# Kernel optimization log

Measured on AMD Instinct MI355X. Metric: run time of the kernel, lower is better.

## Reference

```python
import jax, jax.numpy as jnp
import numpy as np

D_MODEL, N_HEADS = 512, 8
HEAD_DIM = D_MODEL // N_HEADS
LN_EPS = 1e-5


def setup_inputs() -> dict:
    key = jax.random.key(0)
    ks = jax.random.split(key, 6)
    b, n = 8, 1024
    x = jax.random.normal(ks[0], (b, n, D_MODEL), dtype=jnp.float32)
    W_qkv = jax.random.normal(ks[1], (D_MODEL, 3 * D_MODEL), dtype=jnp.float32) * (1.0 / np.sqrt(D_MODEL))
    b_qkv = jnp.zeros((3 * D_MODEL,), dtype=jnp.float32)
    reattn_w = jax.random.normal(ks[2], (N_HEADS, N_HEADS), dtype=jnp.float32)
    ln_g = jnp.ones((N_HEADS,), dtype=jnp.float32)
    ln_b = jnp.zeros((N_HEADS,), dtype=jnp.float32)
    W_out = jax.random.normal(ks[3], (D_MODEL, D_MODEL), dtype=jnp.float32) * (1.0 / np.sqrt(D_MODEL))
    b_out = jnp.zeros((D_MODEL,), dtype=jnp.float32)
    return {"x": x, "W_qkv": W_qkv, "b_qkv": b_qkv, "reattn_w": reattn_w,
            "ln_g": ln_g, "ln_b": ln_b, "W_out": W_out, "b_out": b_out}


def reference(x, W_qkv, b_qkv, reattn_w, ln_g, ln_b, W_out, b_out):
    b, n, _ = x.shape
    scale = jnp.float32(HEAD_DIM ** -0.5)  # lsa=False -> non-trainable constant
    qkv = x @ W_qkv + b_qkv                                  # (b, n, 3*d_model)
    q, k, v = jnp.split(qkv, 3, axis=-1)
    def to_heads(t):  # b n (h d) -> b h n d
        return t.reshape(b, n, N_HEADS, HEAD_DIM).transpose(0, 2, 1, 3)
    q, k, v = to_heads(q), to_heads(k), to_heads(v)
    scores = jnp.einsum('bhid,bhjd->bhij', q, k) * scale      # (b, h, n, n)
    attn = jax.nn.softmax(scores, axis=-1)
    # cross-head re-attention mix
    attn = jnp.einsum('bhij,hk->bkij', attn, reattn_w)
    # LayerNorm over the head axis (axis=1)
    mu = jnp.mean(attn, axis=1, keepdims=True)
    var = jnp.var(attn, axis=1, keepdims=True)
    attn = (attn - mu) * jax.lax.rsqrt(var + LN_EPS)
    attn = attn * ln_g[None, :, None, None] + ln_b[None, :, None, None]
    out = jnp.einsum('bhij,bhjd->bhid', attn, v)              # (b, h, n, d)
    out = out.transpose(0, 2, 1, 3).reshape(b, n, D_MODEL)    # b n (h d)
    out = out @ W_out + b_out
    return (out, attn)
```

## Files before the change

### kernel.cpp

```cpp
#include <hip/hip_runtime.h>

#define SCALE_ 0.125f
#define LN_EPS_ 1e-5f

typedef __attribute__((ext_vector_type(8))) short bf16x8;
typedef __attribute__((ext_vector_type(4))) float f32x4;

__device__ __forceinline__ ushort f2b(float f) {
  union { float f; unsigned u; } x; x.f = f;
  unsigned r = x.u + 0x7FFFu + ((x.u >> 16) & 1u);
  return (ushort)(r >> 16);
}

__device__ __forceinline__ f32x4 mfma16(bf16x8 a, bf16x8 b, f32x4 c) {
  return __builtin_amdgcn_mfma_f32_16x16x32_bf16(a, b, c, 0, 0, 0);
}

__device__ __forceinline__ void bar_lds() {
  asm volatile("s_waitcnt lgkmcnt(0)\n\ts_barrier" ::: "memory");
  __builtin_amdgcn_sched_barrier(0);
}

__global__ __launch_bounds__(256) void cast_transpose(const float* __restrict__ src,
                                                      ushort* __restrict__ dst,
                                                      int R, int C) {
  __shared__ ushort t[64][65];
  const int tid = threadIdx.x;
  const int c0 = blockIdx.x * 64, r0 = blockIdx.y * 64;
  const int lr = tid >> 2, lc = (tid & 3) * 16;
#pragma unroll
  for (int u = 0; u < 4; ++u) {
    float4 v = *(const float4*)&src[(size_t)(r0 + lr) * C + c0 + lc + u * 4];
    t[lc + u * 4 + 0][lr] = f2b(v.x);
    t[lc + u * 4 + 1][lr] = f2b(v.y);
    t[lc + u * 4 + 2][lr] = f2b(v.z);
    t[lc + u * 4 + 3][lr] = f2b(v.w);
  }
  __syncthreads();
#pragma unroll
  for (int u = 0; u < 2; ++u) {
    bf16x8 o;
#pragma unroll
    for (int e = 0; e < 8; ++e) o[e] = (short)t[lr][lc + u * 8 + e];
    *(bf16x8*)&dst[(size_t)(c0 + lr) * R + r0 + lc + u * 8] = o;
  }
}

__global__ __launch_bounds__(256) void qkv_mfma(const float* __restrict__ x,
                                                const ushort* __restrict__ Wt,
                                                const float* __restrict__ bias,
                                                ushort* __restrict__ q,
                                                ushort* __restrict__ k,
                                                ushort* __restrict__ vt) {
  __shared__ ushort A[128][40];
  __shared__ ushort Bs[128][40];
  const int tid = threadIdx.x;
  const int n0 = blockIdx.x * 128;
  const int m0 = blockIdx.y * 128;
  const int lane = tid & 63, wid = tid >> 6;
  const int wr = wid >> 1, wc = wid & 1;
  const int lr = lane & 15, g4 = lane >> 4;
  const int sr = tid >> 1, sco = (tid & 1) * 16;
  f32x4 acc[4][4] = {};
  for (int k0 = 0; k0 < 512; k0 += 32) {
    {
      const float4* xs = (const float4*)&x[(size_t)(m0 + sr) * 512 + k0 + sco];
      float4 v0 = xs[0], v1 = xs[1], v2 = xs[2], v3 = xs[3];
      bf16x8 p0, p1;
      p0[0] = (short)f2b(v0.x); p0[1] = (short)f2b(v0.y);
      p0[2] = (short)f2b(v0.z); p0[3] = (short)f2b(v0.w);
      p0[4] = (short)f2b(v1.x); p0[5] = (short)f2b(v1.y);
      p0[6] = (short)f2b(v1.z); p0[7] = (short)f2b(v1.w);
      p1[0] = (short)f2b(v2.x); p1[1] = (short)f2b(v2.y);
      p1[2] = (short)f2b(v2.z); p1[3] = (short)f2b(v2.w);
      p1[4] = (short)f2b(v3.x); p1[5] = (short)f2b(v3.y);
      p1[6] = (short)f2b(v3.z); p1[7] = (short)f2b(v3.w);
      *(bf16x8*)&A[sr][sco] = p0;
      *(bf16x8*)&A[sr][sco + 8] = p1;
    }
    {
      const bf16x8* wp = (const bf16x8*)&Wt[(size_t)(n0 + sr) * 512 + k0 + sco];
      *(bf16x8*)&Bs[sr][sco] = wp[0];
      *(bf16x8*)&Bs[sr][sco + 8] = wp[1];
    }
    __syncthreads();
    bf16x8 af[4], bf[4];
#pragma unroll
    for (int mr = 0; mr < 4; ++mr) af[mr] = *(bf16x8*)&A[wr * 64 + mr * 16 + lr][g4 * 8];
#pragma unroll
    for (int nr = 0; nr < 4; ++nr) bf[nr] = *(bf16x8*)&Bs[wc * 64 + nr * 16 + lr][g4 * 8];
#pragma unroll
    for (int mr = 0; mr < 4; ++mr)
#pragma unroll
      for (int nr = 0; nr < 4; ++nr) acc[mr][nr] = mfma16(af[mr], bf[nr], acc[mr][nr]);
    __syncthreads();
  }
  const int part = n0 >> 9;
#pragma unroll
  for (int mr = 0; mr < 4; ++mr)
#pragma unroll
    for (int nr = 0; nr < 4; ++nr) {
      const int n = n0 + wc * 64 + nr * 16 + lr;
      const int h = (n & 511) >> 6, d = n & 63;
      const float bb = bias[n];
#pragma unroll
      for (int r = 0; r < 4; ++r) {
        int token = m0 + wr * 64 + mr * 16 + g4 * 4 + r;
        int bi = token >> 10, ii = token & 1023;
        ushort valb = f2b(acc[mr][nr][r] + bb);
        if (part == 0)
          q[(((size_t)(bi * 8 + h) * 1024 + ii) * 64) + d] = valb;
        else if (part == 1)
          k[(((size_t)(bi * 8 + h) * 1024 + ii) * 64) + d] = valb;
        else
          vt[((size_t)(bi * 8 + h) * 64 + d) * 1024 + ii] = valb;
      }
    }
}

__global__ __launch_bounds__(512, 2) void attn_fused(const ushort* __restrict__ q,
                                                     const ushort* __restrict__ k,
                                                     const ushort* __restrict__ vt,
                                                     const float* __restrict__ rw,
                                                     const float* __restrict__ ln_g,
                                                     const float* __restrict__ ln_b,
                                                     float* __restrict__ attn,
                                                     ushort* __restrict__ pv) {
  __shared__ float PM[8][32][36];
  __shared__ float wsh[64];
  __shared__ float gsh[8], bsh[8];

  const int tid = threadIdx.x;
  const int lane = tid & 63;
  const int h = tid >> 6;
  const int obid = ((blockIdx.x & 7) << 5) + (blockIdx.x >> 3);
  const int i0 = (obid & 31) * 32;
  const int b = obid >> 5;
  const int lr = lane & 15, g4 = lane >> 4;

  const ushort* qh = q + ((size_t)(b * 8 + h) * 1024 + i0) * 64;
  const ushort* kh = k + (size_t)(b * 8 + h) * 65536;
  const ushort* vth = vt + (size_t)(b * 8 + h) * 65536;

  if (tid < 64) wsh[tid] = rw[tid];
  if (tid < 8) { gsh[tid] = ln_g[tid]; bsh[tid] = ln_b[tid]; }

  bf16x8 qf[2][2];
#pragma unroll
  for (int mr = 0; mr < 2; ++mr)
#pragma unroll
    for (int ks = 0; ks < 2; ++ks)
      qf[mr][ks] = *(const bf16x8*)&qh[(size_t)(mr * 16 + lr) * 64 + ks * 32 + g4 * 8];

  float psum[2][4] = {};
  {
    bf16x8 kc[4], kn[4];
#pragma unroll
    for (int nr = 0; nr < 2; ++nr)
#pragma unroll
      for (int ks = 0; ks < 2; ++ks)
        kc[nr * 2 + ks] = *(const bf16x8*)&kh[(size_t)(nr * 16 + lr) * 64 + ks * 32 + g4 * 8];
    for (int jt = 0; jt < 32; ++jt) {
      const int j0n = ((jt + 1) & 31) * 32;
#pragma unroll
      for (int nr = 0; nr < 2; ++nr)
#pragma unroll
        for (int ks = 0; ks < 2; ++ks)
          kn[nr * 2 + ks] =
              *(const bf16x8*)&kh[(size_t)(j0n + nr * 16 + lr) * 64 + ks * 32 + g4 * 8];
      f32x4 sa[2][2] = {};
#pragma unroll
      for (int mr = 0; mr < 2; ++mr)
#pragma unroll
        for (int nr = 0; nr < 2; ++nr) {
          sa[mr][nr] = mfma16(qf[mr][0], kc[nr * 2 + 0], sa[mr][nr]);
          sa[mr][nr] = mfma16(qf[mr][1], kc[nr * 2 + 1], sa[mr][nr]);
        }
#pragma unroll
      for (int mr = 0; mr < 2; ++mr)
#pragma unroll
        for (int nr = 0; nr < 2; ++nr)
#pragma unroll
          for (int r = 0; r < 4; ++r) psum[mr][r] += __expf(sa[mr][nr][r] * SCALE_);
#pragma unroll
      for (int i = 0; i < 4; ++i) kc[i] = kn[i];
    }
  }
  float inv_[2][4];
#pragma unroll
  for (int mr = 0; mr < 2; ++mr)
#pragma unroll
    for (int r = 0; r < 4; ++r) {
      float s = psum[mr][r];
#pragma unroll
      for (int off = 1; off <= 8; off <<= 1) s += __shfl_xor(s, off);
      inv_[mr][r] = 1.0f / s;
    }

  f32x4 oacc[2][4] = {};
  const int pair = tid & 1, chunk = tid >> 1;
  const int m_ii = chunk >> 3, m_jj = (chunk & 7) * 4;
  const int k2base = pair * 4;

  bf16x8 kc[4], kn[4];
#pragma unroll
  for (int nr = 0; nr < 2; ++nr)
#pragma unroll
    for (int ks = 0; ks < 2; ++ks)
      kc[nr * 2 + ks] = *(const bf16x8*)&kh[(size_t)(nr * 16 + lr) * 64 + ks * 32 + g4 * 8];

  for (int jt = 0; jt < 32; ++jt) {
    const int j0 = jt * 32;
    const int j0n = ((jt + 1) & 31) * 32;
#pragma unroll
    for (int nr = 0; nr < 2; ++nr)
#pragma unroll
      for (int ks = 0; ks < 2; ++ks)
        kn[nr * 2 + ks] =
            *(const bf16x8*)&kh[(size_t)(j0n + nr * 16 + lr) * 64 + ks * 32 + g4 * 8];

    f32x4 sa[2][2] = {};
#pragma unroll
    for (int mr = 0; mr < 2; ++mr)
#pragma unroll
      for (int nr = 0; nr < 2; ++nr) {
        sa[mr][nr] = mfma16(qf[mr][0], kc[nr * 2 + 0], sa[mr][nr]);
        sa[mr][nr] = mfma16(qf[mr][1], kc[nr * 2 + 1], sa[mr][nr]);
      }
#pragma unroll
    for (int mr = 0; mr < 2; ++mr)
#pragma unroll
      for (int nr = 0; nr < 2; ++nr)
#pragma unroll
        for (int r = 0; r < 4; ++r)
          PM[h][mr * 16 + g4 * 4 + r][nr * 16 + lr] =
              __expf(sa[mr][nr][r] * SCALE_) * inv_[mr][r];

    bf16x8 vc[4];
#pragma unroll
    for (int nd = 0; nd < 4; ++nd)
      vc[nd] = *(const bf16x8*)&vth[(size_t)(nd * 16 + lr) * 1024 + j0 + g4 * 8];

    bar_lds();

    float4 ph[8];
#pragma unroll
    for (int h2 = 0; h2 < 8; ++h2) ph[h2] = *(const float4*)&PM[h2][m_ii][m_jj];
    float mixed[4][4];
#pragma unroll
    for (int k2l = 0; k2l < 4; ++k2l) {
      float a0 = 0.f, a1 = 0.f, a2 = 0.f, a3 = 0.f;
#pragma unroll
      for (int h2 = 0; h2 < 8; ++h2) {
        float w = wsh[h2 * 8 + k2base + k2l];
        a0 += ph[h2].x * w; a1 += ph[h2].y * w;
        a2 += ph[h2].z * w; a3 += ph[h2].w * w;
      }
      mixed[k2l][0] = a0; mixed[k2l][1] = a1; mixed[k2l][2] = a2; mixed[k2l][3] = a3;
    }
    float mu[4], rs_[4];
#pragma unroll
    for (int e = 0; e < 4; ++e) {
      float mp = mixed[0][e] + mixed[1][e] + mixed[2][e] + mixed[3][e];
      mu[e] = (mp + __shfl_xor(mp, 1)) * 0.125f;
    }
#pragma unroll
    for (int e = 0; e < 4; ++e) {
      float vp = 0.f;
#pragma unroll
      for (int k2l = 0; k2l < 4; ++k2l) {
        float d = mixed[k2l][e] - mu[e];
        vp += d * d;
      }
      float var = (vp + __shfl_xor(vp, 1)) * 0.125f;
      rs_[e] = rsqrtf(var + LN_EPS_);
    }
#pragma unroll
    for (int k2l = 0; k2l < 4; ++k2l) {
      int k2 = k2base + k2l;
      float g = gsh[k2], be = bsh[k2];
      f32x4 o;
      o[0] = (mixed[k2l][0] - mu[0]) * rs_[0] * g + be;
      o[1] = (mixed[k2l][1] - mu[1]) * rs_[1] * g + be;
      o[2] = (mixed[k2l][2] - mu[2]) * rs_[2] * g + be;
      o[3] = (mixed[k2l][3] - mu[3]) * rs_[3] * g + be;
      __builtin_nontemporal_store(
          o, (f32x4*)&attn[((size_t)(b * 8 + k2) << 20) + ((size_t)(i0 + m_ii) << 10) +
                           j0 + m_jj]);
      *(f32x4*)&PM[k2][m_ii][m_jj] = o;
    }

    bar_lds();

    bf16x8 pa[2];
#pragma unroll
    for (int mr = 0; mr < 2; ++mr) {
      const float* pr = &PM[h][mr * 16 + lr][g4 * 8];
      float4 p0 = *(const float4*)&pr[0];
      float4 p1 = *(const float4*)&pr[4];
      bf16x8 t;
      t[0] = (short)f2b(p0.x); t[1] = (short)f2b(p0.y);
      t[2] = (short)f2b(p0.z); t[3] = (short)f2b(p0.w);
      t[4] = (short)f2b(p1.x); t[5] = (short)f2b(p1.y);
      t[6] = (short)f2b(p1.z); t[7] = (short)f2b(p1.w);
      pa[mr] = t;
    }
#pragma unroll
    for (int nd = 0; nd < 4; ++nd) {
      oacc[0][nd] = mfma16(pa[0], vc[nd], oacc[0][nd]);
      oacc[1][nd] = mfma16(pa[1], vc[nd], oacc[1][nd]);
    }

#pragma unroll
    for (int i = 0; i < 4; ++i) kc[i] = kn[i];
  }

  ushort* po = pv + ((size_t)(b * 8 + h) * 1024 + i0) * 64;
#pragma unroll
  for (int mr = 0; mr < 2; ++mr)
#pragma unroll
    for (int nd = 0; nd < 4; ++nd)
#pragma unroll
      for (int r = 0; r < 4; ++r)
        po[(size_t)(mr * 16 + g4 * 4 + r) * 64 + nd * 16 + lr] = f2b(oacc[mr][nd][r]);
}

__global__ __launch_bounds__(256) void out_mfma(const ushort* __restrict__ pvb,
                                                const ushort* __restrict__ Wt,
                                                const float* __restrict__ bias,
                                                float* __restrict__ out) {
  __shared__ ushort A[128][40];
  __shared__ ushort Bs[128][40];
  const int tid = threadIdx.x;
  const int n0 = blockIdx.x * 128;
  const int m0 = blockIdx.y * 128;
  const int lane = tid & 63, wid = tid >> 6;
  const int wr = wid >> 1, wc = wid & 1;
  const int lr = lane & 15, g4 = lane >> 4;
  const int sr = tid >> 1, sco = (tid & 1) * 16;
  f32x4 acc[4][4] = {};
  for (int k0 = 0; k0 < 512; k0 += 32) {
    {
      int token = m0 + sr;
      int bi = token >> 10, ii = token & 1023;
      int f = k0 + sco;
      int hh = f >> 6, d = f & 63;
      const bf16x8* src =
          (const bf16x8*)&pvb[(((size_t)(bi * 8 + hh)) * 1024 + ii) * 64 + d];
      *(bf16x8*)&A[sr][sco] = src[0];
      *(bf16x8*)&A[sr][sco + 8] = src[1];
    }
    {
      const bf16x8* wp = (const bf16x8*)&Wt[(size_t)(n0 + sr) * 512 + k0 + sco];
      *(bf16x8*)&Bs[sr][sco] = wp[0];
      *(bf16x8*)&Bs[sr][sco + 8] = wp[1];
    }
    __syncthreads();
    bf16x8 af[4], bf[4];
#pragma unroll
    for (int mr = 0; mr < 4; ++mr) af[mr] = *(bf16x8*)&A[wr * 64 + mr * 16 + lr][g4 * 8];
#pragma unroll
    for (int nr = 0; nr < 4; ++nr) bf[nr] = *(bf16x8*)&Bs[wc * 64 + nr * 16 + lr][g4 * 8];
#pragma unroll
    for (int mr = 0; mr < 4; ++mr)
#pragma unroll
      for (int nr = 0; nr < 4; ++nr) acc[mr][nr] = mfma16(af[mr], bf[nr], acc[mr][nr]);
    __syncthreads();
  }
#pragma unroll
  for (int mr = 0; mr < 4; ++mr)
#pragma unroll
    for (int nr = 0; nr < 4; ++nr) {
      const int n = n0 + wc * 64 + nr * 16 + lr;
      const float bb = bias[n];
#pragma unroll
      for (int r = 0; r < 4; ++r) {
        int token = m0 + wr * 64 + mr * 16 + g4 * 4 + r;
        out[(size_t)token * 512 + n] = acc[mr][nr][r] + bb;
      }
    }
}

extern "C" void kernel_launch(void* const* d_in, const int* in_sizes, int n_in,
                              void* d_out, int out_size, void* d_ws, size_t ws_size,
                              hipStream_t stream) {
  const float* x    = (const float*)d_in[0];
  const float* Wqkv = (const float*)d_in[1];
  const float* bqkv = (const float*)d_in[2];
  const float* rw   = (const float*)d_in[3];
  const float* lng  = (const float*)d_in[4];
  const float* lnb  = (const float*)d_in[5];
  const float* Wout = (const float*)d_in[6];
  const float* bout = (const float*)d_in[7];

  float* out  = (float*)d_out;
  float* attn = (float*)d_out + 4194304;

  char* wsb = (char*)d_ws;
  ushort* q     = (ushort*)(wsb);
  ushort* k     = (ushort*)(wsb + (8u << 20));
  ushort* vt    = (ushort*)(wsb + (16u << 20));
  ushort* pvb   = (ushort*)(wsb + (24u << 20));
  ushort* Wqkvt = (ushort*)(wsb + (32u << 20));
  ushort* Woutt = (ushort*)(wsb + (33u << 20) + (1u << 19));

  cast_transpose<<<dim3(24, 8), 256, 0, stream>>>(Wqkv, Wqkvt, 512, 1536);
  cast_transpose<<<dim3(8, 8), 256, 0, stream>>>(Wout, Woutt, 512, 512);

  qkv_mfma<<<dim3(12, 64), 256, 0, stream>>>(x, Wqkvt, bqkv, q, k, vt);
  attn_fused<<<dim3(256), 512, 0, stream>>>(q, k, vt, rw, lng, lnb, attn, pvb);
  out_mfma<<<dim3(4, 64), 256, 0, stream>>>(pvb, Woutt, bout, out);
}
```

Before: 183.6 us.

## Split softmax denominators into separate kernel and halve attention key range per block

Moves the softmax row-sum pass out of the fused attention kernel into a new small kernel that writes per-row inverse denominators. The fused kernel then only does one pass over half the key range per block, doubling the grid to 512 blocks. The two partial P·V results go to separate bf16 buffers that out_mfma sums on load. It also transposes the MFMA operand order for vectorized LDS and global stores and uses a packed bf16 conversion. This targets the low block count of the old grid and the duplicated QK^T pass. The cost is an extra launch, extra workspace traffic, and an added bf16 rounding from summing two partial results.

```diff
diff --git a/kernel.cpp b/kernel.cpp
--- a/kernel.cpp
+++ b/kernel.cpp
@@ -1,4 +1,5 @@
 #include <hip/hip_runtime.h>
+#include <hip/hip_bf16.h>
 
 #define SCALE_ 0.125f
 #define LN_EPS_ 1e-5f
@@ -10,6 +11,14 @@
   union { float f; unsigned u; } x; x.f = f;
   unsigned r = x.u + 0x7FFFu + ((x.u >> 16) & 1u);
   return (ushort)(r >> 16);
+}
+__device__ __forceinline__ float b2f(short s) {
+  union { float f; unsigned u; } x; x.u = ((unsigned)(ushort)s) << 16; return x.f;
+}
+__device__ __forceinline__ unsigned cvtpk(float lo, float hi) {
+  union { __hip_bfloat162 h; unsigned u; } x;
+  x.h = __float22bfloat162_rn(make_float2(lo, hi));
+  return x.u;
 }
 
 __device__ __forceinline__ f32x4 mfma16(bf16x8 a, bf16x8 b, f32x4 c) {
@@ -118,14 +127,80 @@
     }
 }
 
-__global__ __launch_bounds__(512, 2) void attn_fused(const ushort* __restrict__ q,
+__global__ __launch_bounds__(64) void denoms(const ushort* __restrict__ q,
+                                             const ushort* __restrict__ k,
+                                             float* __restrict__ invg) {
+  const int bid = blockIdx.x;
+  const int obid = ((bid & 7) << 8) + (bid >> 3);
+  const int bh = obid >> 5;
+  const int it = obid & 31;
+  const int lane = threadIdx.x;
+  const int lr = lane & 15, g4 = lane >> 4;
+  const ushort* qh = q + ((size_t)bh * 1024 + it * 32) * 64;
+  const ushort* kh = k + (size_t)bh * 65536;
+
+  bf16x8 qf[2][2];
+#pragma unroll
+  for (int ir = 0; ir < 2; ++ir)
+#pragma unroll
+    for (int ks = 0; ks < 2; ++ks)
+      qf[ir][ks] = *(const bf16x8*)&qh[(size_t)(ir * 16 + lr) * 64 + ks * 32 + g4 * 8];
+
+  float psum[2] = {0.f, 0.f};
+  bf16x8 kc[4], kn[4];
+#pragma unroll
+  for (int jr = 0; jr < 2; ++jr)
+#pragma unroll
+    for (int ks = 0; ks < 2; ++ks)
+      kc[jr * 2 + ks] = *(const bf16x8*)&kh[(size_t)(jr * 16 + lr) * 64 + ks * 32 + g4 * 8];
+  for (int jt = 0; jt < 32; ++jt) {
+    const int j0n = ((jt + 1) & 31) * 32;
+#pragma unroll
+    for (int jr = 0; jr < 2; ++jr)
+#pragma unroll
+      for (int ks = 0; ks < 2; ++ks)
+        kn[jr * 2 + ks] =
+            *(const bf16x8*)&kh[(size_t)(j0n + jr * 16 + lr) * 64 + ks * 32 + g4 * 8];
+    f32x4 sa[2][2] = {};
+#pragma unroll
+    for (int jr = 0; jr < 2; ++jr)
+#pragma unroll
+      for (int ir = 0; ir < 2; ++ir) {
+        sa[jr][ir] = mfma16(kc[jr * 2 + 0], qf[ir][0], sa[jr][ir]);
+        sa[jr][ir] = mfma16(kc[jr * 2 + 1], qf[ir][1], sa[jr][ir]);
+      }
+#pragma unroll
+    for (int jr = 0; jr < 2; ++jr)
+#pragma unroll
+      for (int ir = 0; ir < 2; ++ir)
+#pragma unroll
+        for (int r = 0; r < 4; ++r) psum[ir] += __expf(sa[jr][ir][r] * SCALE_);
+#pragma unroll
+    for (int i = 0; i < 4; ++i) kc[i] = kn[i];
+  }
+#pragma unroll
+  for (int ir = 0; ir < 2; ++ir) {
+    float s = psum[ir];
+    s += __shfl_xor(s, 16);
+    s += __shfl_xor(s, 32);
+    psum[ir] = s;
+  }
+  if (lane < 16) {
+    invg[(size_t)bh * 1024 + it * 32 + lr] = 1.0f / psum[0];
+    invg[(size_t)bh * 1024 + it * 32 + 16 + lr] = 1.0f / psum[1];
+  }
+}
+
+__global__ __launch_bounds__(512, 4) void attn_fused(const ushort* __restrict__ q,
                                                      const ushort* __restrict__ k,
                                                      const ushort* __restrict__ vt,
                                                      const float* __restrict__ rw,
                                                      const float* __restrict__ ln_g,
                                                      const float* __restrict__ ln_b,
+                                                     const float* __restrict__ invg,
                                                      float* __restrict__ attn,
-                                                     ushort* __restrict__ pv) {
+                                                     ushort* __restrict__ pv0,
+                                                     ushort* __restrict__ pv1) {
   __shared__ float PM[8][32][36];
   __shared__ float wsh[64];
   __shared__ float gsh[8], bsh[8];
@@ -133,113 +208,71 @@
   const int tid = threadIdx.x;
   const int lane = tid & 63;
   const int h = tid >> 6;
-  const int obid = ((blockIdx.x & 7) << 5) + (blockIdx.x >> 3);
-  const int i0 = (obid & 31) * 32;
-  const int b = obid >> 5;
+  const int obid = ((blockIdx.x & 7) << 6) + (blockIdx.x >> 3);
+  const int b = obid >> 6;
+  const int rem = obid & 63;
+  const int i0 = (rem & 31) * 32;
+  const int jh = rem >> 5;
+  const int jbase = jh * 512;
   const int lr = lane & 15, g4 = lane >> 4;
 
-  const ushort* qh = q + ((size_t)(b * 8 + h) * 1024 + i0) * 64;
-  const ushort* kh = k + (size_t)(b * 8 + h) * 65536;
-  const ushort* vth = vt + (size_t)(b * 8 + h) * 65536;
+  const int bh = b * 8 + h;
+  const ushort* qh = q + ((size_t)bh * 1024 + i0) * 64;
+  const ushort* kh = k + (size_t)bh * 65536;
+  const ushort* vth = vt + (size_t)bh * 65536;
 
   if (tid < 64) wsh[tid] = rw[tid];
   if (tid < 8) { gsh[tid] = ln_g[tid]; bsh[tid] = ln_b[tid]; }
 
   bf16x8 qf[2][2];
 #pragma unroll
-  for (int mr = 0; mr < 2; ++mr)
+  for (int ir = 0; ir < 2; ++ir)
 #pragma unroll
     for (int ks = 0; ks < 2; ++ks)
-      qf[mr][ks] = *(const bf16x8*)&qh[(size_t)(mr * 16 + lr) * 64 + ks * 32 + g4 * 8];
-
-  float psum[2][4] = {};
-  {
-    bf16x8 kc[4], kn[4];
-#pragma unroll
-    for (int nr = 0; nr < 2; ++nr)
-#pragma unroll
-      for (int ks = 0; ks < 2; ++ks)
-        kc[nr * 2 + ks] = *(const bf16x8*)&kh[(size_t)(nr * 16 + lr) * 64 + ks * 32 + g4 * 8];
-    for (int jt = 0; jt < 32; ++jt) {
-      const int j0n = ((jt + 1) & 31) * 32;
-#pragma unroll
-      for (int nr = 0; nr < 2; ++nr)
-#pragma unroll
-        for (int ks = 0; ks < 2; ++ks)
-          kn[nr * 2 + ks] =
-              *(const bf16x8*)&kh[(size_t)(j0n + nr * 16 + lr) * 64 + ks * 32 + g4 * 8];
-      f32x4 sa[2][2] = {};
-#pragma unroll
-      for (int mr = 0; mr < 2; ++mr)
-#pragma unroll
-        for (int nr = 0; nr < 2; ++nr) {
-          sa[mr][nr] = mfma16(qf[mr][0], kc[nr * 2 + 0], sa[mr][nr]);
-          sa[mr][nr] = mfma16(qf[mr][1], kc[nr * 2 + 1], sa[mr][nr]);
-        }
-#pragma unroll
-      for (int mr = 0; mr < 2; ++mr)
-#pragma unroll
-        for (int nr = 0; nr < 2; ++nr)
-#pragma unroll
-          for (int r = 0; r < 4; ++r) psum[mr][r] += __expf(sa[mr][nr][r] * SCALE_);
-#pragma unroll
-      for (int i = 0; i < 4; ++i) kc[i] = kn[i];
-    }
-  }
-  float inv_[2][4];
-#pragma unroll
-  for (int mr = 0; mr < 2; ++mr)
-#pragma unroll
-    for (int r = 0; r < 4; ++r) {
-      float s = psum[mr][r];
-#pragma unroll
-      for (int off = 1; off <= 8; off <<= 1) s += __shfl_xor(s, off);
-      inv_[mr][r] = 1.0f / s;
-    }
-
-  f32x4 oacc[2][4] = {};
+      qf[ir][ks] = *(const bf16x8*)&qh[(size_t)(ir * 16 + lr) * 64 + ks * 32 + g4 * 8];
+
+  float invv[2];
+#pragma unroll
+  for (int ir = 0; ir < 2; ++ir)
+    invv[ir] = invg[(size_t)bh * 1024 + i0 + ir * 16 + lr];
+
+  f32x4 oaccT[4][2] = {};
   const int pair = tid & 1, chunk = tid >> 1;
   const int m_ii = chunk >> 3, m_jj = (chunk & 7) * 4;
   const int k2base = pair * 4;
 
-  bf16x8 kc[4], kn[4];
-#pragma unroll
-  for (int nr = 0; nr < 2; ++nr)
-#pragma unroll
-    for (int ks = 0; ks < 2; ++ks)
-      kc[nr * 2 + ks] = *(const bf16x8*)&kh[(size_t)(nr * 16 + lr) * 64 + ks * 32 + g4 * 8];
-
-  for (int jt = 0; jt < 32; ++jt) {
-    const int j0 = jt * 32;
-    const int j0n = ((jt + 1) & 31) * 32;
-#pragma unroll
-    for (int nr = 0; nr < 2; ++nr)
+  for (int jt = 0; jt < 16; ++jt) {
+    const int j0 = jbase + jt * 32;
+    bf16x8 kf[4];
+#pragma unroll
+    for (int jr = 0; jr < 2; ++jr)
 #pragma unroll
       for (int ks = 0; ks < 2; ++ks)
-        kn[nr * 2 + ks] =
-            *(const bf16x8*)&kh[(size_t)(j0n + nr * 16 + lr) * 64 + ks * 32 + g4 * 8];
+        kf[jr * 2 + ks] =
+            *(const bf16x8*)&kh[(size_t)(j0 + jr * 16 + lr) * 64 + ks * 32 + g4 * 8];
 
     f32x4 sa[2][2] = {};
 #pragma unroll
-    for (int mr = 0; mr < 2; ++mr)
-#pragma unroll
-      for (int nr = 0; nr < 2; ++nr) {
-        sa[mr][nr] = mfma16(qf[mr][0], kc[nr * 2 + 0], sa[mr][nr]);
-        sa[mr][nr] = mfma16(qf[mr][1], kc[nr * 2 + 1], sa[mr][nr]);
-      }
-#pragma unroll
-    for (int mr = 0; mr < 2; ++mr)
-#pragma unroll
-      for (int nr = 0; nr < 2; ++nr)
-#pragma unroll
-        for (int r = 0; r < 4; ++r)
-          PM[h][mr * 16 + g4 * 4 + r][nr * 16 + lr] =
-              __expf(sa[mr][nr][r] * SCALE_) * inv_[mr][r];
+    for (int jr = 0; jr < 2; ++jr)
+#pragma unroll
+      for (int ir = 0; ir < 2; ++ir) {
+        sa[jr][ir] = mfma16(kf[jr * 2 + 0], qf[ir][0], sa[jr][ir]);
+        sa[jr][ir] = mfma16(kf[jr * 2 + 1], qf[ir][1], sa[jr][ir]);
+      }
+#pragma unroll
+    for (int jr = 0; jr < 2; ++jr)
+#pragma unroll
+      for (int ir = 0; ir < 2; ++ir) {
+        f32x4 pw;
+#pragma unroll
+        for (int r = 0; r < 4; ++r) pw[r] = __expf(sa[jr][ir][r] * SCALE_) * invv[ir];
+        *(f32x4*)&PM[h][ir * 16 + lr][jr * 16 + g4 * 4] = pw;
+      }
 
     bf16x8 vc[4];
 #pragma unroll
-    for (int nd = 0; nd < 4; ++nd)
-      vc[nd] = *(const bf16x8*)&vth[(size_t)(nd * 16 + lr) * 1024 + j0 + g4 * 8];
+    for (int dr = 0; dr < 4; ++dr)
+      vc[dr] = *(const bf16x8*)&vth[(size_t)(dr * 16 + lr) * 1024 + j0 + g4 * 8];
 
     bar_lds();
 
@@ -292,40 +325,40 @@
 
     bar_lds();
 
-    bf16x8 pa[2];
-#pragma unroll
-    for (int mr = 0; mr < 2; ++mr) {
-      const float* pr = &PM[h][mr * 16 + lr][g4 * 8];
+    bf16x8 pab[2];
+#pragma unroll
+    for (int ic = 0; ic < 2; ++ic) {
+      const float* pr = &PM[h][ic * 16 + lr][g4 * 8];
       float4 p0 = *(const float4*)&pr[0];
       float4 p1 = *(const float4*)&pr[4];
-      bf16x8 t;
-      t[0] = (short)f2b(p0.x); t[1] = (short)f2b(p0.y);
-      t[2] = (short)f2b(p0.z); t[3] = (short)f2b(p0.w);
-      t[4] = (short)f2b(p1.x); t[5] = (short)f2b(p1.y);
-      t[6] = (short)f2b(p1.z); t[7] = (short)f2b(p1.w);
-      pa[mr] = t;
-    }
-#pragma unroll
-    for (int nd = 0; nd < 4; ++nd) {
-      oacc[0][nd] = mfma16(pa[0], vc[nd], oacc[0][nd]);
-      oacc[1][nd] = mfma16(pa[1], vc[nd], oacc[1][nd]);
-    }
-
-#pragma unroll
-    for (int i = 0; i < 4; ++i) kc[i] = kn[i];
-  }
-
-  ushort* po = pv + ((size_t)(b * 8 + h) * 1024 + i0) * 64;
-#pragma unroll
-  for (int mr = 0; mr < 2; ++mr)
-#pragma unroll
-    for (int nd = 0; nd < 4; ++nd)
-#pragma unroll
-      for (int r = 0; r < 4; ++r)
-        po[(size_t)(mr * 16 + g4 * 4 + r) * 64 + nd * 16 + lr] = f2b(oacc[mr][nd][r]);
-}
-
-__global__ __launch_bounds__(256) void out_mfma(const ushort* __restrict__ pvb,
+      union { bf16x8 v; unsigned u[4]; } pk;
+      pk.u[0] = cvtpk(p0.x, p0.y);
+      pk.u[1] = cvtpk(p0.z, p0.w);
+      pk.u[2] = cvtpk(p1.x, p1.y);
+      pk.u[3] = cvtpk(p1.z, p1.w);
+      pab[ic] = pk.v;
+    }
+#pragma unroll
+    for (int dr = 0; dr < 4; ++dr) {
+      oaccT[dr][0] = mfma16(vc[dr], pab[0], oaccT[dr][0]);
+      oaccT[dr][1] = mfma16(vc[dr], pab[1], oaccT[dr][1]);
+    }
+  }
+
+  ushort* po = (jh == 0 ? pv0 : pv1) + ((size_t)bh * 1024 + i0) * 64;
+#pragma unroll
+  for (int ic = 0; ic < 2; ++ic)
+#pragma unroll
+    for (int dr = 0; dr < 4; ++dr) {
+      union { ushort4 s; unsigned u[2]; } o;
+      o.u[0] = cvtpk(oaccT[dr][ic][0], oaccT[dr][ic][1]);
+      o.u[1] = cvtpk(oaccT[dr][ic][2], oaccT[dr][ic][3]);
+      *(ushort4*)&po[(size_t)(ic * 16 + lr) * 64 + dr * 16 + g4 * 4] = o.s;
+    }
+}
+
+__global__ __launch_bounds__(256) void out_mfma(const ushort* __restrict__ pv0,
+                                                const ushort* __restrict__ pv1,
                                                 const ushort* __restrict__ Wt,
                                                 const float* __restrict__ bias,
                                                 float* __restrict__ out) {
@@ -345,10 +378,19 @@
       int bi = token >> 10, ii = token & 1023;
       int f = k0 + sco;
       int hh = f >> 6, d = f & 63;
-      const bf16x8* src =
-          (const bf16x8*)&pvb[(((size_t)(bi * 8 + hh)) * 1024 + ii) * 64 + d];
-      *(bf16x8*)&A[sr][sco] = src[0];
-      *(bf16x8*)&A[sr][sco + 8] = src[1];
+      const size_t idx = (((size_t)(bi * 8 + hh)) * 1024 + ii) * 64 + d;
+      bf16x8 a0 = *(const bf16x8*)&pv0[idx];
+      bf16x8 a1 = *(const bf16x8*)&pv0[idx + 8];
+      bf16x8 c0 = *(const bf16x8*)&pv1[idx];
+      bf16x8 c1 = *(const bf16x8*)&pv1[idx + 8];
+      bf16x8 r0, r1;
+#pragma unroll
+      for (int e = 0; e < 8; ++e) {
+        r0[e] = (short)f2b(b2f(a0[e]) + b2f(c0[e]));
+        r1[e] = (short)f2b(b2f(a1[e]) + b2f(c1[e]));
+      }
+      *(bf16x8*)&A[sr][sco] = r0;
+      *(bf16x8*)&A[sr][sco + 8] = r1;
     }
     {
       const bf16x8* wp = (const bf16x8*)&Wt[(size_t)(n0 + sr) * 512 + k0 + sco];
@@ -400,14 +442,17 @@
   ushort* q     = (ushort*)(wsb);
   ushort* k     = (ushort*)(wsb + (8u << 20));
   ushort* vt    = (ushort*)(wsb + (16u << 20));
-  ushort* pvb   = (ushort*)(wsb + (24u << 20));
-  ushort* Wqkvt = (ushort*)(wsb + (32u << 20));
-  ushort* Woutt = (ushort*)(wsb + (33u << 20) + (1u << 19));
+  ushort* pv0   = (ushort*)(wsb + (24u << 20));
+  ushort* pv1   = (ushort*)(wsb + (32u << 20));
+  ushort* Wqkvt = (ushort*)(wsb + (40u << 20));
+  ushort* Woutt = (ushort*)(wsb + (41u << 20) + (1u << 19));
+  float*  invg  = (float*)(wsb + (42u << 20));
 
   cast_transpose<<<dim3(24, 8), 256, 0, stream>>>(Wqkv, Wqkvt, 512, 1536);
   cast_transpose<<<dim3(8, 8), 256, 0, stream>>>(Wout, Woutt, 512, 512);
 
   qkv_mfma<<<dim3(12, 64), 256, 0, stream>>>(x, Wqkvt, bqkv, q, k, vt);
-  attn_fused<<<dim3(256), 512, 0, stream>>>(q, k, vt, rw, lng, lnb, attn, pvb);
-  out_mfma<<<dim3(4, 64), 256, 0, stream>>>(pvb, Woutt, bout, out);
-}
+  denoms<<<dim3(2048), 64, 0, stream>>>(q, k, invg);
+  attn_fused<<<dim3(512), 512, 0, stream>>>(q, k, vt, rw, lng, lnb, invg, attn, pv0, pv1);
+  out_mfma<<<dim3(4, 64), 256, 0, stream>>>(pv0, pv1, Woutt, bout, out);
+}
```

Result: slower. 329.2 us (+79.3%).
